# Optimization experiments

Measured on AMD Instinct MI355X. Metric: run time of the kernel, lower is better.

Reference implementation:

```python
import jax, jax.numpy as jnp
import numpy as np

EMBED_DIM = 1024
NUM_HEADS = 16
HEAD_DIM = 64
B, S = 4, 2048


def setup_inputs() -> dict:
    key = jax.random.key(0)
    ks = jax.random.split(key, 5)
    std = 0.02
    x = jax.random.normal(ks[0], (B, S, EMBED_DIM), dtype=jnp.float32)
    Wq = std * jax.random.normal(ks[1], (NUM_HEADS, EMBED_DIM, HEAD_DIM), dtype=jnp.float32)
    Wk = std * jax.random.normal(ks[2], (NUM_HEADS, EMBED_DIM, HEAD_DIM), dtype=jnp.float32)
    Wv = std * jax.random.normal(ks[3], (NUM_HEADS, EMBED_DIM, HEAD_DIM), dtype=jnp.float32)
    Wo = std * jax.random.normal(ks[4], (NUM_HEADS, HEAD_DIM, EMBED_DIM), dtype=jnp.float32)
    bq = jnp.zeros((NUM_HEADS, HEAD_DIM), dtype=jnp.float32)
    bk = jnp.zeros((NUM_HEADS, HEAD_DIM), dtype=jnp.float32)
    bv = jnp.zeros((NUM_HEADS, HEAD_DIM), dtype=jnp.float32)
    bo = jnp.zeros((EMBED_DIM,), dtype=jnp.float32)
    return {"x": x, "Wq": Wq, "bq": bq, "Wk": Wk, "bk": bk,
            "Wv": Wv, "bv": bv, "Wo": Wo, "bo": bo}


def reference(x, Wq, bq, Wk, bk, Wv, bv, Wo, bo):
    # q,k,v: [b, s, n, h]
    q = jnp.einsum('bsd,ndh->bsnh', x, Wq) + bq
    k = jnp.einsum('bsd,ndh->bsnh', x, Wk) + bk
    v = jnp.einsum('bsd,ndh->bsnh', x, Wv) + bv
    scale = 1.0 / (HEAD_DIM ** 0.5)
    # non-causal full attention matrix [b, n, s, t]
    attn = jnp.einsum('bsnh,btnh->bnst', q, k) * scale
    attn = jax.nn.softmax(attn, axis=-1)
    after = jnp.einsum('bnst,btnh->bsnh', attn, v)
    out = jnp.einsum('bsnh,nhd->bsd', after, Wo) + bo
    return out
```

## Files before the change

### kernel.cpp

```cpp
#include <hip/hip_runtime.h>

typedef __bf16 bf16;
typedef bf16 bf16x8 __attribute__((ext_vector_type(8)));
typedef bf16 bf16x4 __attribute__((ext_vector_type(4)));
typedef bf16 bf16x2 __attribute__((ext_vector_type(2)));
typedef float f32x4 __attribute__((ext_vector_type(4)));
typedef float f32x16 __attribute__((ext_vector_type(16)));
typedef unsigned int u32;
typedef u32 u32x4 __attribute__((ext_vector_type(4)));
typedef int i32x2 __attribute__((ext_vector_type(2)));

constexpr int Bb = 4, Ss = 2048, Dd = 1024, NH = 16, HD = 64;
constexpr int BS = Bb * Ss;
constexpr float CSC = 0.18033688011112042f;

__device__ __forceinline__ int sw(int row, int col) {
  return (row << 6) + (col ^ ((row & 7) << 3));
}
__device__ __forceinline__ int sw128(int row, int col) {
  return (row << 7) + (col ^ ((row & 7) << 3));
}

__device__ __forceinline__ void g2l16(const bf16* g, bf16* l) {
  __builtin_amdgcn_global_load_lds(
      (const __attribute__((address_space(1))) void*)g,
      (__attribute__((address_space(3))) void*)l, 16, 0, 0);
}

__device__ __forceinline__ u32 pkbf(float a, float b) {
  bf16x2 v = {(bf16)a, (bf16)b};
  return __builtin_bit_cast(u32, v);
}

__global__ void prep(const float* __restrict__ x, bf16* __restrict__ xb,
                     const float* __restrict__ Wq, const float* __restrict__ Wk,
                     const float* __restrict__ Wv, const float* __restrict__ Wo,
                     const float* __restrict__ bq, const float* __restrict__ bk,
                     const float* __restrict__ bv,
                     bf16* __restrict__ WT_all, bf16* __restrict__ WoT,
                     float* __restrict__ bias_all) {
  __shared__ bf16 Ts[64 * 72];
  const int t = threadIdx.x;
  if (blockIdx.y == 0) {
    int o = (blockIdx.x * 256 + t) * 4;
    f32x4 v = *(const f32x4*)&x[o];
    bf16x4 r = {(bf16)v[0], (bf16)v[1], (bf16)v[2], (bf16)v[3]};
    *(bf16x4*)&xb[o] = r;
    return;
  }
  if (blockIdx.x > 1024) return;
  if (blockIdx.x == 1024) {
    for (int j = t; j < 3072; j += 256) {
      int s2 = j >> 10;
      const float* bb = (s2 == 0) ? bq : (s2 == 1) ? bk : bv;
      bias_all[j] = bb[j & 1023] * (s2 == 0 ? CSC : 1.0f);
    }
    return;
  }
  const int sel = blockIdx.x >> 8, bx = blockIdx.x & 255;
  if (sel < 3) {
    const float* W = (sel == 0) ? Wq : (sel == 1) ? Wk : Wv;
    float scale = (sel == 0) ? CSC : 1.0f;
    int head = bx >> 4, dt = bx & 15;
    const float* src = W + head * 65536 + dt * 64 * 64;
#pragma unroll
    for (int i = 0; i < 4; ++i) {
      int idx = i * 256 + t;
      int dr = idx >> 4, hc = (idx & 15) * 4;
      f32x4 v = *(const f32x4*)&src[dr * 64 + hc];
#pragma unroll
      for (int k = 0; k < 4; ++k) Ts[(hc + k) * 72 + dr] = (bf16)(v[k] * scale);
    }
    __syncthreads();
    bf16* dst = WT_all + (size_t)sel * 1048576 + (size_t)(head * 64) * 1024 + dt * 64;
#pragma unroll
    for (int i = 0; i < 2; ++i) {
      int idx = i * 256 + t;
      int hr = idx >> 3, ch = (idx & 7) * 8;
      *(bf16x8*)&dst[(size_t)hr * 1024 + ch] = *(const bf16x8*)&Ts[hr * 72 + ch];
    }
  } else {
    int ct = bx >> 4, dt = bx & 15;
    const float* src = Wo + (size_t)(ct * 64) * 1024 + dt * 64;
#pragma unroll
    for (int i = 0; i < 4; ++i) {
      int idx = i * 256 + t;
      int cr = idx >> 4, dc = (idx & 15) * 4;
      f32x4 v = *(const f32x4*)&src[(size_t)cr * 1024 + dc];
#pragma unroll
      for (int k = 0; k < 4; ++k) Ts[(dc + k) * 72 + cr] = (bf16)v[k];
    }
    __syncthreads();
    bf16* dst = WoT + (size_t)(dt * 64) * 1024 + ct * 64;
#pragma unroll
    for (int i = 0; i < 2; ++i) {
      int idx = i * 256 + t;
      int dr = idx >> 3, ch = (idx & 7) * 8;
      *(bf16x8*)&dst[(size_t)dr * 1024 + ch] = *(const bf16x8*)&Ts[dr * 72 + ch];
    }
  }
}

__device__ __forceinline__ void gemm_core(const bf16* __restrict__ A,
                                          const bf16* __restrict__ BT,
                                          int m0, int n0, bf16* As, bf16* Bs,
                                          f32x4 (&acc)[4][4]) {
  const int t = threadIdx.x;
  const int l = t & 63, q = l >> 4, lm = l & 15;
  const int w = t >> 6, wm = w & 1, wn = w >> 1;
  int ro[4], co[4];
#pragma unroll
  for (int i = 0; i < 4; ++i) {
    int o = i * 256 + t;
    ro[i] = o >> 3;
    co[i] = ((o & 7) ^ ((o >> 3) & 7)) << 3;
  }
  const int lbase = (t & 192) * 8;
  for (int k0 = 0; k0 < 1024; k0 += 64) {
    __syncthreads();
#pragma unroll
    for (int i = 0; i < 4; ++i)
      g2l16(&A[(size_t)(m0 + ro[i]) * 1024 + k0 + co[i]], &As[i * 2048 + lbase]);
#pragma unroll
    for (int i = 0; i < 4; ++i)
      g2l16(&BT[(size_t)(n0 + ro[i]) * 1024 + k0 + co[i]], &Bs[i * 2048 + lbase]);
    __syncthreads();
#pragma unroll
    for (int kh = 0; kh < 2; ++kh) {
      bf16x8 a[4], b[4];
#pragma unroll
      for (int i = 0; i < 4; ++i)
        a[i] = *(const bf16x8*)&As[sw(wm * 64 + i * 16 + lm, kh * 32 + q * 8)];
#pragma unroll
      for (int i = 0; i < 4; ++i)
        b[i] = *(const bf16x8*)&Bs[sw(wn * 64 + i * 16 + lm, kh * 32 + q * 8)];
#pragma unroll
      for (int mt = 0; mt < 4; ++mt)
#pragma unroll
        for (int nt = 0; nt < 4; ++nt)
          acc[mt][nt] = __builtin_amdgcn_mfma_f32_16x16x32_bf16(a[mt], b[nt], acc[mt][nt], 0, 0, 0);
    }
  }
}

__global__ __launch_bounds__(512, 2) void gemm_qk8(const bf16* __restrict__ A,
                                                   const bf16* __restrict__ BT,
                                                   const float* __restrict__ bias_all,
                                                   bf16* __restrict__ C) {
  __shared__ __align__(16) bf16 SMEM[65536];
  const int t = threadIdx.x;
  const int l = t & 63, q = l >> 4, lm = l & 15;
  const int w = t >> 6, wm = w & 1, wn = w >> 1;
  const int bid = blockIdx.x;
  const int xcd = bid & 7, cc = bid >> 3;
  const int mt = xcd * 4 + (cc >> 3), nt = cc & 7;
  const int m0 = mt * 256, n0 = nt * 256;
  const bf16* Ag = A + (size_t)m0 * 1024;
  const bf16* Bg = BT + (size_t)n0 * 1024;
  const int sR = t >> 3;
  const int sC = t & 7;
  const int dstb = (t & 448) * 8;

  auto stA = [&](int bufb, int h, int kt) {
#pragma unroll
    for (int i = 0; i < 2; ++i) {
      int Lh = i * 64 + sR;
      int gr = ((Lh >> 6) << 7) + h * 64 + (Lh & 63);
      g2l16(&Ag[(size_t)gr * 1024 + kt * 64 + ((sC ^ (Lh & 7)) << 3)],
            &SMEM[bufb * 32768 + h * 8192 + i * 4096 + dstb]);
    }
  };
  auto stB = [&](int bufb, int h, int kt) {
#pragma unroll
    for (int i = 0; i < 2; ++i) {
      int Lh = i * 64 + sR;
      int gr = ((Lh >> 5) << 6) + h * 32 + (Lh & 31);
      g2l16(&Bg[(size_t)gr * 1024 + kt * 64 + ((sC ^ (Lh & 7)) << 3)],
            &SMEM[bufb * 32768 + 16384 + h * 8192 + i * 4096 + dstb]);
    }
  };
  auto rdA = [&](int base, int mt16, int ks) {
    int L = ((mt16 >> 2) << 7) + wm * 64 + ((mt16 & 3) << 4) + lm;
    return *(const bf16x8*)&SMEM[base + sw(L, ks * 32 + q * 8)];
  };
  auto rdB = [&](int base, int nt16, int ks) {
    int L = ((nt16 >> 1) << 7) + wn * 32 + ((nt16 & 1) << 4) + lm;
    return *(const bf16x8*)&SMEM[base + 16384 + sw(L, ks * 32 + q * 8)];
  };

  stA(0, 0, 0); stA(0, 1, 0); stB(0, 0, 0); stB(0, 1, 0);
  stA(1, 0, 1); stB(1, 0, 1);
  asm volatile("s_waitcnt vmcnt(4)" ::: "memory");
  __builtin_amdgcn_s_barrier();
  __builtin_amdgcn_sched_barrier(0);

  f32x4 acc[8][4] = {};
  int cur = 0;
  for (int kt = 0; kt < 16; ++kt, cur ^= 1) {
    const int base = cur * 32768;
    bf16x8 af[4][2], b0[2][2], b1[2][2];
#pragma unroll
    for (int mi = 0; mi < 4; ++mi)
#pragma unroll
      for (int ks = 0; ks < 2; ++ks) af[mi][ks] = rdA(base, mi, ks);
#pragma unroll
    for (int ni = 0; ni < 2; ++ni)
#pragma unroll
      for (int ks = 0; ks < 2; ++ks) b0[ni][ks] = rdB(base, ni, ks);
    if (kt + 1 < 16) { stA(cur ^ 1, 1, kt + 1); stB(cur ^ 1, 1, kt + 1); }
    __builtin_amdgcn_s_barrier();
    __builtin_amdgcn_s_setprio(1);
#pragma unroll
    for (int mi = 0; mi < 4; ++mi)
#pragma unroll
      for (int ni = 0; ni < 2; ++ni)
#pragma unroll
        for (int ks = 0; ks < 2; ++ks)
          acc[mi][ni] = __builtin_amdgcn_mfma_f32_16x16x32_bf16(af[mi][ks], b0[ni][ks], acc[mi][ni], 0, 0, 0);
    __builtin_amdgcn_s_setprio(0);
    __builtin_amdgcn_sched_barrier(0);
    __builtin_amdgcn_s_barrier();
    __builtin_amdgcn_sched_barrier(0);
#pragma unroll
    for (int ni = 0; ni < 2; ++ni)
#pragma unroll
      for (int ks = 0; ks < 2; ++ks) b1[ni][ks] = rdB(base, 2 + ni, ks);
    __builtin_amdgcn_s_barrier();
    __builtin_amdgcn_s_setprio(1);
#pragma unroll
    for (int mi = 0; mi < 4; ++mi)
#pragma unroll
      for (int ni = 0; ni < 2; ++ni)
#pragma unroll
        for (int ks = 0; ks < 2; ++ks)
          acc[mi][2 + ni] = __builtin_amdgcn_mfma_f32_16x16x32_bf16(af[mi][ks], b1[ni][ks], acc[mi][2 + ni], 0, 0, 0);
    __builtin_amdgcn_s_setprio(0);
    __builtin_amdgcn_sched_barrier(0);
    __builtin_amdgcn_s_barrier();
    __builtin_amdgcn_sched_barrier(0);
#pragma unroll
    for (int mi = 0; mi < 4; ++mi)
#pragma unroll
      for (int ks = 0; ks < 2; ++ks) af[mi][ks] = rdA(base, 4 + mi, ks);
#pragma unroll
    for (int ni = 0; ni < 2; ++ni)
#pragma unroll
      for (int ks = 0; ks < 2; ++ks) b0[ni][ks] = rdB(base, ni, ks);
    if (kt + 2 < 16) stA(cur, 0, kt + 2);
    __builtin_amdgcn_s_barrier();
    __builtin_amdgcn_s_setprio(1);
#pragma unroll
    for (int mi = 0; mi < 4; ++mi)
#pragma unroll
      for (int ni = 0; ni < 2; ++ni)
#pragma unroll
        for (int ks = 0; ks < 2; ++ks)
          acc[4 + mi][ni] = __builtin_amdgcn_mfma_f32_16x16x32_bf16(af[mi][ks], b0[ni][ks], acc[4 + mi][ni], 0, 0, 0);
    __builtin_amdgcn_s_setprio(0);
    __builtin_amdgcn_sched_barrier(0);
    __builtin_amdgcn_s_barrier();
    __builtin_amdgcn_sched_barrier(0);
#pragma unroll
    for (int ni = 0; ni < 2; ++ni)
#pragma unroll
      for (int ks = 0; ks < 2; ++ks) b1[ni][ks] = rdB(base, 2 + ni, ks);
    if (kt + 2 < 16) stB(cur, 0, kt + 2);
    __builtin_amdgcn_s_barrier();
    __builtin_amdgcn_s_setprio(1);
#pragma unroll
    for (int mi = 0; mi < 4; ++mi)
#pragma unroll
      for (int ni = 0; ni < 2; ++ni)
#pragma unroll
        for (int ks = 0; ks < 2; ++ks)
          acc[4 + mi][2 + ni] = __builtin_amdgcn_mfma_f32_16x16x32_bf16(af[mi][ks], b1[ni][ks], acc[4 + mi][2 + ni], 0, 0, 0);
    __builtin_amdgcn_s_setprio(0);
    if (kt == 14) asm volatile("s_waitcnt vmcnt(0)" ::: "memory");
    else          asm volatile("s_waitcnt vmcnt(4)" ::: "memory");
    __builtin_amdgcn_sched_barrier(0);
    __builtin_amdgcn_s_barrier();
    __builtin_amdgcn_sched_barrier(0);
  }
#pragma unroll
  for (int mi = 0; mi < 8; ++mi) {
    int row = m0 + wm * 128 + mi * 16 + q * 4;
#pragma unroll
    for (int ni = 0; ni < 4; ++ni) {
      int col = n0 + wn * 64 + ni * 16 + lm;
      float bb = bias_all[col];
#pragma unroll
      for (int r = 0; r < 4; ++r)
        C[(size_t)(row + r) * 2048 + col] = (bf16)(acc[mi][ni][r] + bb);
    }
  }
}

__global__ __launch_bounds__(256) void gemm_v(const bf16* __restrict__ xb,
                                              const bf16* __restrict__ WT,
                                              const float* __restrict__ bias_all,
                                              bf16* __restrict__ VTb) {
  __shared__ __align__(16) bf16 SMEM[2 * 128 * 64];
  bf16* As = SMEM;
  bf16* Bs = SMEM + 128 * 64;
  const int bid = blockIdx.x;
  const int t = threadIdx.x;
  const int l = t & 63, q = l >> 4, lm = l & 15;
  const int w = t >> 6, wm = w & 1, wn = w >> 1;
  const int xcd = bid & 7, idx = bid >> 3;
  const int m0 = (idx >> 3) * 128;
  const int n0 = (xcd * 8 + (idx & 7)) * 128;
  const bf16* A = WT + (size_t)2048 * 1024;
  const bf16* BT = xb;
  f32x4 acc[4][4] = {};
  gemm_core(A, BT, m0, n0, As, Bs, acc);
  __syncthreads();
#pragma unroll
  for (int nt = 0; nt < 4; ++nt) {
    int sl = wn * 64 + nt * 16 + lm;
#pragma unroll
    for (int mt = 0; mt < 4; ++mt) {
      int ml = wm * 64 + mt * 16 + q * 4;
#pragma unroll
      for (int r = 0; r < 4; ++r)
        SMEM[sw128(ml + r, sl)] = (bf16)(acc[mt][nt][r] + bias_all[2048 + m0 + ml + r]);
    }
  }
  __syncthreads();
  int hh = t >> 1, half = (t & 1) * 64;
  int m = m0 + hh;
  size_t gb = (size_t)((n0 >> 11) * 16 + (m >> 6)) * 131072 +
              (size_t)(m & 63) * 2048 + (n0 & 2047) + half;
#pragma unroll
  for (int k = 0; k < 8; ++k)
    *(bf16x8*)&VTb[gb + k * 8] = *(const bf16x8*)&SMEM[sw128(hh, half + k * 8)];
}

__global__ __launch_bounds__(256) void gemm_out(const bf16* __restrict__ after,
                                                const bf16* __restrict__ WoT,
                                                const float* __restrict__ bo,
                                                float* __restrict__ out) {
  __shared__ __align__(16) bf16 SMEM[2 * 128 * 64];
  const int bid = blockIdx.x;
  const int t = threadIdx.x;
  const int l = t & 63, q = l >> 4, lm = l & 15;
  const int w = t >> 6, wm = w & 1, wn = w >> 1;
  const int xcd = bid & 7, idx = bid >> 3;
  const int n0 = xcd * 128, m0 = idx * 128;
  f32x4 acc[4][4] = {};
  gemm_core(after, WoT, m0, n0, SMEM, SMEM + 128 * 64, acc);
#pragma unroll
  for (int nt = 0; nt < 4; ++nt) {
    int col = n0 + wn * 64 + nt * 16 + lm;
    float bb = bo[col];
#pragma unroll
    for (int mt = 0; mt < 4; ++mt) {
      int row = m0 + wm * 64 + mt * 16 + q * 4;
#pragma unroll
      for (int r = 0; r < 4; ++r)
        out[(size_t)(row + r) * 1024 + col] = acc[mt][nt][r] + bb;
    }
  }
}

__global__ __launch_bounds__(256, 2) void attn(const bf16* __restrict__ QK,
                                               const bf16* __restrict__ VT,
                                               bf16* __restrict__ after) {
  __shared__ __align__(16) bf16 SMEM[32768];
  const int t = threadIdx.x;
  const int l = t & 63, w = t >> 6;
  const int lh = l & 31, H = l >> 5;
  const int f = blockIdx.x;
  const int bn = (f & 7) | ((f >> 6) << 3);
  const int s0 = ((f >> 3) & 7) * 256;
  const int b = bn >> 4, n = bn & 15;
  const bf16* Qb = QK + (size_t)(b * 2048) * 2048 + n * 64;
  const bf16* Kb = Qb + 1024;
  const bf16* Vtb = VT + (size_t)bn * 131072;
  const int rr = t >> 3;
  const int co0 = ((t & 7) ^ (rr & 7)) << 3;
  const int lbase = (t & 192) * 8;
#pragma unroll
  for (int i = 0; i < 8; ++i)
    g2l16(&Qb[(size_t)(s0 + i * 32 + rr) * 2048 + co0], &SMEM[i * 2048 + lbase]);
  __syncthreads();
  bf16x8 qb[2][4];
#pragma unroll
  for (int qt = 0; qt < 2; ++qt)
#pragma unroll
    for (int ks = 0; ks < 4; ++ks)
      qb[qt][ks] = *(const bf16x8*)&SMEM[sw(w * 64 + qt * 32 + lh, ks * 16 + H * 8)];
  __syncthreads();
#pragma unroll
  for (int s = 0; s < 3; ++s)
#pragma unroll
    for (int i = 0; i < 2; ++i) {
      g2l16(&Kb[(size_t)(s * 64 + i * 32 + rr) * 2048 + co0],
            &SMEM[s * 4096 + i * 2048 + lbase]);
      g2l16(&Vtb[(size_t)(i * 32 + rr) * 2048 + s * 64 + co0],
            &SMEM[16384 + s * 4096 + i * 2048 + lbase]);
    }
  f32x16 o_acc[2][2] = {};
  float rsA[2] = {0.f, 0.f}, rsB[2] = {0.f, 0.f};
  for (int rd = 0; rd < 32; ++rd) {
    const int cur = rd & 3;
    const bf16* Ks = &SMEM[cur * 4096];
    const bf16* Vs = &SMEM[16384 + cur * 4096];
    if (rd < 30)       asm volatile("s_waitcnt vmcnt(8)" ::: "memory");
    else if (rd == 30) asm volatile("s_waitcnt vmcnt(4)" ::: "memory");
    else               asm volatile("s_waitcnt vmcnt(0)" ::: "memory");
    __builtin_amdgcn_s_barrier();
    __builtin_amdgcn_sched_barrier(0);
    if (rd <= 28) {
      int st = rd + 3, nb = st & 3, t0n = st * 64;
#pragma unroll
      for (int i = 0; i < 2; ++i) {
        g2l16(&Kb[(size_t)(t0n + i * 32 + rr) * 2048 + co0],
              &SMEM[nb * 4096 + i * 2048 + lbase]);
        g2l16(&Vtb[(size_t)(i * 32 + rr) * 2048 + t0n + co0],
              &SMEM[16384 + nb * 4096 + i * 2048 + lbase]);
      }
    }
#pragma unroll
    for (int tt = 0; tt < 2; ++tt) {
      bf16x8 kb[4];
#pragma unroll
      for (int ks = 0; ks < 4; ++ks)
        kb[ks] = *(const bf16x8*)&Ks[sw(tt * 32 + lh, ks * 16 + H * 8)];
      f32x16 sc[2] = {};
      __builtin_amdgcn_s_setprio(1);
#pragma unroll
      for (int ks = 0; ks < 4; ++ks)
#pragma unroll
        for (int qt = 0; qt < 2; ++qt)
          sc[qt] = __builtin_amdgcn_mfma_f32_32x32x16_bf16(kb[ks], qb[qt][ks], sc[qt], 0, 0, 0);
      __builtin_amdgcn_s_setprio(0);
      u32 pk[2][8];
#pragma unroll
      for (int qt = 0; qt < 2; ++qt)
#pragma unroll
        for (int i = 0; i < 8; ++i) {
          float p0 = __builtin_amdgcn_exp2f(sc[qt][2 * i]);
          float p1 = __builtin_amdgcn_exp2f(sc[qt][2 * i + 1]);
          rsA[qt] += p0;
          rsB[qt] += p1;
          pk[qt][i] = pkbf(p0, p1);
        }
#pragma unroll
      for (int ks2 = 0; ks2 < 2; ++ks2) {
        bf16x8 pa[2];
#pragma unroll
        for (int qt = 0; qt < 2; ++qt) {
          u32x4 av;
#if __has_builtin(__builtin_amdgcn_permlane32_swap)
          i32x2 sA = __builtin_amdgcn_permlane32_swap(
              (int)pk[qt][ks2 * 4 + 0], (int)pk[qt][ks2 * 4 + 2], false, false);
          i32x2 sB = __builtin_amdgcn_permlane32_swap(
              (int)pk[qt][ks2 * 4 + 1], (int)pk[qt][ks2 * 4 + 3], false, false);
          av[0] = (u32)sA[0]; av[1] = (u32)sB[0]; av[2] = (u32)sA[1]; av[3] = (u32)sB[1];
#else
          u32 xx[4];
          xx[0] = __shfl_xor((int)pk[qt][ks2 * 4 + 0], 32);
          xx[1] = __shfl_xor((int)pk[qt][ks2 * 4 + 1], 32);
          xx[2] = __shfl_xor((int)pk[qt][ks2 * 4 + 2], 32);
          xx[3] = __shfl_xor((int)pk[qt][ks2 * 4 + 3], 32);
          av[0] = H ? xx[2] : pk[qt][ks2 * 4 + 0];
          av[1] = H ? xx[3] : pk[qt][ks2 * 4 + 1];
          av[2] = H ? pk[qt][ks2 * 4 + 2] : xx[0];
          av[3] = H ? pk[qt][ks2 * 4 + 3] : xx[1];
#endif
          pa[qt] = __builtin_bit_cast(bf16x8, av);
        }
        __builtin_amdgcn_s_setprio(1);
#pragma unroll
        for (int ht = 0; ht < 2; ++ht) {
          bf16x8 vb = *(const bf16x8*)&Vs[sw(ht * 32 + lh, tt * 32 + ks2 * 16 + H * 8)];
#pragma unroll
          for (int qt = 0; qt < 2; ++qt)
            o_acc[qt][ht] = __builtin_amdgcn_mfma_f32_32x32x16_bf16(pa[qt], vb, o_acc[qt][ht], 0, 0, 0);
        }
        __builtin_amdgcn_s_setprio(0);
      }
    }
  }
#pragma unroll
  for (int qt = 0; qt < 2; ++qt) {
    float rs = rsA[qt] + rsB[qt];
    rs += __shfl_xor(rs, 32);
    float inv = 1.f / rs;
#pragma unroll
    for (int r = 0; r < 16; ++r) {
      int sl = (r & 3) + 8 * (r >> 2) + 4 * H;
      float invr = __shfl(inv, sl);
      size_t base = (size_t)(b * 2048 + s0 + w * 64 + qt * 32 + sl) * 1024 + n * 64;
#pragma unroll
      for (int ht = 0; ht < 2; ++ht)
        after[base + ht * 32 + lh] = (bf16)(o_acc[qt][ht][r] * invr);
    }
  }
}

extern "C" void kernel_launch(void* const* d_in, const int* in_sizes, int n_in,
                              void* d_out, int out_size, void* d_ws, size_t ws_size,
                              hipStream_t stream) {
  const float* x  = (const float*)d_in[0];
  const float* Wq = (const float*)d_in[1];
  const float* bq = (const float*)d_in[2];
  const float* Wk = (const float*)d_in[3];
  const float* bk = (const float*)d_in[4];
  const float* Wv = (const float*)d_in[5];
  const float* bv = (const float*)d_in[6];
  const float* Wo = (const float*)d_in[7];
  const float* bo = (const float*)d_in[8];
  float* out = (float*)d_out;

  bf16* WT_all    = (bf16*)d_ws;
  bf16* WoT       = WT_all + (size_t)3072 * 1024;
  float* bias_all = (float*)(WoT + (size_t)1024 * 1024);
  bf16* xb        = (bf16*)(bias_all + 4096);
  bf16* QKb       = xb + (size_t)BS * Dd;
  bf16* VTb       = QKb + (size_t)BS * 2048;
  bf16* after     = VTb + (size_t)Bb * NH * HD * Ss;

  prep<<<dim3(8192, 2), dim3(256), 0, stream>>>(x, xb, Wq, Wk, Wv, Wo, bq, bk, bv,
                                                WT_all, WoT, bias_all);
  gemm_v<<<dim3(512), dim3(256), 0, stream>>>(xb, WT_all, bias_all, VTb);
  gemm_qk8<<<dim3(256), dim3(512), 0, stream>>>(xb, WT_all, bias_all, QKb);
  attn<<<dim3(512), dim3(256), 0, stream>>>(QKb, VTb, after);
  gemm_out<<<dim3(512), dim3(256), 0, stream>>>(after, WoT, bo, out);
}
```

Baseline: 272.2 us.

## Merge V projection GEMM into QK GEMM launch as extra blocks

Fuses the separate V-projection kernel into the QK projection kernel by adding 256 extra 512-thread blocks. Each extra block runs two independent 256-thread V tiles, one per half, on separate shared-memory regions. This removes one kernel launch and lets V and QK tiles share the device at the same time, avoiding the tail of each kernel. The V blocks now run under the QK kernel's launch bounds (512 threads, 2 blocks per CU) and its 128KB shared allocation. The block-wide __syncthreads inside the V path also couples the two halves, which may change occupancy.

Result: faster. 266.7 us (-2.0%).

```diff
diff --git a/kernel.cpp b/kernel.cpp
--- a/kernel.cpp
+++ b/kernel.cpp
@@ -101,21 +101,20 @@
   }
 }
 
-__device__ __forceinline__ void gemm_core(const bf16* __restrict__ A,
-                                          const bf16* __restrict__ BT,
-                                          int m0, int n0, bf16* As, bf16* Bs,
-                                          f32x4 (&acc)[4][4]) {
-  const int t = threadIdx.x;
-  const int l = t & 63, q = l >> 4, lm = l & 15;
-  const int w = t >> 6, wm = w & 1, wn = w >> 1;
+__device__ __forceinline__ void gemm_core_t(int tl, const bf16* __restrict__ A,
+                                            const bf16* __restrict__ BT,
+                                            int m0, int n0, bf16* As, bf16* Bs,
+                                            f32x4 (&acc)[4][4]) {
+  const int l = tl & 63, q = l >> 4, lm = l & 15;
+  const int w = tl >> 6, wm = w & 1, wn = w >> 1;
   int ro[4], co[4];
 #pragma unroll
   for (int i = 0; i < 4; ++i) {
-    int o = i * 256 + t;
+    int o = i * 256 + tl;
     ro[i] = o >> 3;
     co[i] = ((o & 7) ^ ((o >> 3) & 7)) << 3;
   }
-  const int lbase = (t & 192) * 8;
+  const int lbase = (tl & 192) * 8;
   for (int k0 = 0; k0 < 1024; k0 += 64) {
     __syncthreads();
 #pragma unroll
@@ -143,15 +142,52 @@
   }
 }
 
-__global__ __launch_bounds__(512, 2) void gemm_qk8(const bf16* __restrict__ A,
+__global__ __launch_bounds__(512, 2) void gemm_vqk(const bf16* __restrict__ A,
                                                    const bf16* __restrict__ BT,
                                                    const float* __restrict__ bias_all,
-                                                   bf16* __restrict__ C) {
+                                                   bf16* __restrict__ QKb,
+                                                   bf16* __restrict__ VTb) {
   __shared__ __align__(16) bf16 SMEM[65536];
+  const int bid = blockIdx.x;
   const int t = threadIdx.x;
+  if (bid >= 256) {
+    const int vh = t >> 8;
+    const int tl = t & 255;
+    bf16* As = SMEM + vh * 16384;
+    bf16* Bs = As + 8192;
+    const int vbid = (bid - 256) + vh * 256;
+    const int xcd = vbid & 7, idx = vbid >> 3;
+    const int m0 = (idx >> 3) * 128;
+    const int n0 = (xcd * 8 + (idx & 7)) * 128;
+    const bf16* Av = BT + (size_t)2048 * 1024;
+    const int l = tl & 63, q = l >> 4, lm = l & 15;
+    const int w = tl >> 6, wm = w & 1, wn = w >> 1;
+    f32x4 acc[4][4] = {};
+    gemm_core_t(tl, Av, A, m0, n0, As, Bs, acc);
+    __syncthreads();
+#pragma unroll
+    for (int nt = 0; nt < 4; ++nt) {
+      int sl = wn * 64 + nt * 16 + lm;
+#pragma unroll
+      for (int mt = 0; mt < 4; ++mt) {
+        int ml = wm * 64 + mt * 16 + q * 4;
+#pragma unroll
+        for (int r = 0; r < 4; ++r)
+          As[sw128(ml + r, sl)] = (bf16)(acc[mt][nt][r] + bias_all[2048 + m0 + ml + r]);
+      }
+    }
+    __syncthreads();
+    int hh = tl >> 1, half = (tl & 1) * 64;
+    int m = m0 + hh;
+    size_t gb = (size_t)((n0 >> 11) * 16 + (m >> 6)) * 131072 +
+                (size_t)(m & 63) * 2048 + (n0 & 2047) + half;
+#pragma unroll
+    for (int k = 0; k < 8; ++k)
+      *(bf16x8*)&VTb[gb + k * 8] = *(const bf16x8*)&As[sw128(hh, half + k * 8)];
+    return;
+  }
   const int l = t & 63, q = l >> 4, lm = l & 15;
   const int w = t >> 6, wm = w & 1, wn = w >> 1;
-  const int bid = blockIdx.x;
   const int xcd = bid & 7, cc = bid >> 3;
   const int mt = xcd * 4 + (cc >> 3), nt = cc & 7;
   const int m0 = mt * 256, n0 = nt * 256;
@@ -290,49 +326,9 @@
       float bb = bias_all[col];
 #pragma unroll
       for (int r = 0; r < 4; ++r)
-        C[(size_t)(row + r) * 2048 + col] = (bf16)(acc[mi][ni][r] + bb);
-    }
-  }
-}
-
-__global__ __launch_bounds__(256) void gemm_v(const bf16* __restrict__ xb,
-                                              const bf16* __restrict__ WT,
-                                              const float* __restrict__ bias_all,
-                                              bf16* __restrict__ VTb) {
-  __shared__ __align__(16) bf16 SMEM[2 * 128 * 64];
-  bf16* As = SMEM;
-  bf16* Bs = SMEM + 128 * 64;
-  const int bid = blockIdx.x;
-  const int t = threadIdx.x;
-  const int l = t & 63, q = l >> 4, lm = l & 15;
-  const int w = t >> 6, wm = w & 1, wn = w >> 1;
-  const int xcd = bid & 7, idx = bid >> 3;
-  const int m0 = (idx >> 3) * 128;
-  const int n0 = (xcd * 8 + (idx & 7)) * 128;
-  const bf16* A = WT + (size_t)2048 * 1024;
-  const bf16* BT = xb;
-  f32x4 acc[4][4] = {};
-  gemm_core(A, BT, m0, n0, As, Bs, acc);
-  __syncthreads();
-#pragma unroll
-  for (int nt = 0; nt < 4; ++nt) {
-    int sl = wn * 64 + nt * 16 + lm;
-#pragma unroll
-    for (int mt = 0; mt < 4; ++mt) {
-      int ml = wm * 64 + mt * 16 + q * 4;
-#pragma unroll
-      for (int r = 0; r < 4; ++r)
-        SMEM[sw128(ml + r, sl)] = (bf16)(acc[mt][nt][r] + bias_all[2048 + m0 + ml + r]);
-    }
-  }
-  __syncthreads();
-  int hh = t >> 1, half = (t & 1) * 64;
-  int m = m0 + hh;
-  size_t gb = (size_t)((n0 >> 11) * 16 + (m >> 6)) * 131072 +
-              (size_t)(m & 63) * 2048 + (n0 & 2047) + half;
-#pragma unroll
-  for (int k = 0; k < 8; ++k)
-    *(bf16x8*)&VTb[gb + k * 8] = *(const bf16x8*)&SMEM[sw128(hh, half + k * 8)];
+        QKb[(size_t)(row + r) * 2048 + col] = (bf16)(acc[mi][ni][r] + bb);
+    }
+  }
 }
 
 __global__ __launch_bounds__(256) void gemm_out(const bf16* __restrict__ after,
@@ -347,7 +343,7 @@
   const int xcd = bid & 7, idx = bid >> 3;
   const int n0 = xcd * 128, m0 = idx * 128;
   f32x4 acc[4][4] = {};
-  gemm_core(after, WoT, m0, n0, SMEM, SMEM + 128 * 64, acc);
+  gemm_core_t(t, after, WoT, m0, n0, SMEM, SMEM + 128 * 64, acc);
 #pragma unroll
   for (int nt = 0; nt < 4; ++nt) {
     int col = n0 + wn * 64 + nt * 16 + lm;
@@ -523,8 +519,7 @@
 
   prep<<<dim3(8192, 2), dim3(256), 0, stream>>>(x, xb, Wq, Wk, Wv, Wo, bq, bk, bv,
                                                 WT_all, WoT, bias_all);
-  gemm_v<<<dim3(512), dim3(256), 0, stream>>>(xb, WT_all, bias_all, VTb);
-  gemm_qk8<<<dim3(256), dim3(512), 0, stream>>>(xb, WT_all, bias_all, QKb);
+  gemm_vqk<<<dim3(512), dim3(512), 0, stream>>>(xb, WT_all, bias_all, QKb, VTb);
   attn<<<dim3(512), dim3(256), 0, stream>>>(QKb, VTb, after);
   gemm_out<<<dim3(512), dim3(256), 0, stream>>>(after, WoT, bo, out);
 }
```
